# Performance work log

Hardware: AMD Instinct MI355X
Metric: run time of the kernel (lower is better)

The kernel has to match this reference:

```python
import jax, jax.numpy as jnp
import numpy as np

SOFTMAX = True
SPLAT = True


def setup_inputs() -> dict:
    key = jax.random.key(0)
    k1, k2 = jax.random.split(key)
    data = jax.random.normal(k1, (4, 3, 128, 128), dtype=jnp.float32)
    kernels = jax.random.normal(k2, (4, 441, 128, 128), dtype=jnp.float32)
    return {"data": data, "kernels": kernels}


def _scatter2gather(kern):
    # kern: [bs, k, k, h, w] splat kernels. Gather weight at pixel p for
    # neighbor offset d equals splat weight at pixel p+d for offset -d:
    #   gather[b,i,j,y,x] = splat[b, k-1-i, k-1-j, y+i-c, x+j-c]  (zero outside)
    bs, k, _, h, w = kern.shape
    c = k // 2
    flipped = kern[:, ::-1, ::-1]  # [bs,k,k,h,w]
    padded = jnp.pad(flipped, ((0, 0), (0, 0), (0, 0), (c, c), (c, c)))
    idx = jnp.arange(k)

    def slice_ij(i, j):
        plane = padded[:, i, j]  # [bs, h+2c, w+2c]
        return jax.lax.dynamic_slice(plane, (0, i, j), (bs, h, w))

    g = jax.vmap(lambda i: jax.vmap(lambda j: slice_ij(i, j))(idx))(idx)  # [k,k,bs,h,w]
    return jnp.transpose(g, (2, 0, 1, 3, 4))


def _kernel_weighting(data, kern):
    # out[b,c,y,x] = sum_ij kern[b,i,j,y,x] * data[b,c,y+i-cc,x+j-cc] (zero pad)
    # sum_w = same filtering applied to an all-ones tensor.
    bs, ch, h, w = data.shape
    k = kern.shape[1]
    cc = k // 2
    patches = jax.lax.conv_general_dilated_patches(
        data, (k, k), (1, 1), ((cc, cc), (cc, cc)))  # [bs, ch*k*k, h, w]
    patches = patches.reshape(bs, ch, k, k, h, w)
    out = jnp.einsum('bcijyx,bijyx->bcyx', patches, kern)
    # validity mask = zero-padded ones, separable in y/x
    ii = jnp.arange(k)
    yy = jnp.arange(h)
    xx = jnp.arange(w)
    py = yy[None, :] + ii[:, None] - cc  # [k,h]
    px = xx[None, :] + ii[:, None] - cc  # [k,w]
    vy = ((py >= 0) & (py < h))
    vx = ((px >= 0) & (px < w))
    valid = (vy[:, None, :, None] & vx[None, :, None, :]).astype(kern.dtype)  # [k,k,h,w]
    sum_w = jnp.einsum('bijyx,ijyx->byx', kern, valid)
    return out, sum_w


def reference(data, kernels):
    bs, k2, h, w = kernels.shape
    k = int(np.sqrt(k2))
    kern = kernels.reshape(bs, k, k, h, w)
    if SPLAT:
        kern = _scatter2gather(kern)
    if SOFTMAX:
        kern = jax.nn.softmax(kern.reshape(bs, k * k, h, w), axis=1)
        kern = kern.reshape(bs, k, k, h, w)
    out, sum_w = _kernel_weighting(data, kern)
    return out, sum_w[:, None]  # [bs,ch,h,w], [bs,1,h,w]
```

## Files before the change

kernel.cpp:

```cpp
#include <hip/hip_runtime.h>

#define KS 21
#define CC 10
#define H 128
#define W 128
#define HW (H*W)
#define NCH 3
#define B 4
#define PW (W + 2*CC)

typedef _Float16 half4v __attribute__((ext_vector_type(4)));
struct __attribute__((packed)) f4u { float v[4]; };

#define DT_BYTES (21*PW*8)

__global__ __launch_bounds__(256, 2)
void kaw_gather(const float* __restrict__ data,
                const float* __restrict__ kern,
                float* __restrict__ out,
                float* __restrict__ sumw)
{
    __shared__ __align__(16) unsigned char smem[DT_BYTES];
    unsigned char* dtB = smem;

    const int tid = threadIdx.x;
    const int w = tid & 7;
    const int t = tid >> 3;
    const int y = blockIdx.x;
    const int b = blockIdx.y;

    const float* __restrict__ kbase = kern + (size_t)b * (KS * KS) * HW;
    const float* __restrict__ dbase = data + (size_t)b * NCH * HW;

    for (int e = tid; e < 21 * PW; e += 256) {
        int r  = (e * 7085) >> 20;
        int c  = e - r * PW;
        int gy = y + r - CC;
        int gx = c - CC;
        half4v v = (half4v){(_Float16)0, (_Float16)0, (_Float16)0, (_Float16)0};
        if ((unsigned)gy < (unsigned)H && (unsigned)gx < (unsigned)W) {
            v.x = (_Float16)dbase[(0 * H + gy) * W + gx];
            v.y = (_Float16)dbase[(1 * H + gy) * W + gx];
            v.z = (_Float16)dbase[(2 * H + gy) * W + gx];
        }
        *reinterpret_cast<half4v*>(dtB + e * 8) = v;
    }
    __syncthreads();

    float a00 = 0.f, a01 = 0.f, a02 = 0.f, aw0 = 0.f;
    float a10 = 0.f, a11 = 0.f, a12 = 0.f, aw1 = 0.f;
    float a20 = 0.f, a21 = 0.f, a22 = 0.f, aw2 = 0.f;
    float a30 = 0.f, a31 = 0.f, a32 = 0.f, aw3 = 0.f;

    const int ntap = (w == 0) ? 56 : 55;
    int T = w;
    #pragma unroll 4
    for (int k = 0; k < ntap; ++k, T += 8) {
        int i  = (T * 3121) >> 16;
        int j  = T - i * 21;
        int py = y + i - CC;
        bool rv = (unsigned)py < (unsigned)H;
        int pyc = py < 0 ? 0 : (py > H - 1 ? H - 1 : py);
        int c0 = 4 * t + j - CC;
        f4u g = *reinterpret_cast<const f4u*>(
            kbase + (((440 - T) << 14) + (pyc << 7) + c0));
        float e0 = (rv && (unsigned)(c0 + 0) < (unsigned)W) ? __expf(g.v[0]) : 0.f;
        float e1 = (rv && (unsigned)(c0 + 1) < (unsigned)W) ? __expf(g.v[1]) : 0.f;
        float e2 = (rv && (unsigned)(c0 + 2) < (unsigned)W) ? __expf(g.v[2]) : 0.f;
        float e3 = (rv && (unsigned)(c0 + 3) < (unsigned)W) ? __expf(g.v[3]) : 0.f;
        const unsigned char* dp = dtB + (unsigned)(i * PW + c0 + CC) * 8;
        half4v d0 = *reinterpret_cast<const half4v*>(dp +  0);
        half4v d1 = *reinterpret_cast<const half4v*>(dp +  8);
        half4v d2 = *reinterpret_cast<const half4v*>(dp + 16);
        half4v d3 = *reinterpret_cast<const half4v*>(dp + 24);
        a00 += e0 * (float)d0.x; a01 += e0 * (float)d0.y; a02 += e0 * (float)d0.z; aw0 += e0;
        a10 += e1 * (float)d1.x; a11 += e1 * (float)d1.y; a12 += e1 * (float)d1.z; aw1 += e1;
        a20 += e2 * (float)d2.x; a21 += e2 * (float)d2.y; a22 += e2 * (float)d2.z; aw2 += e2;
        a30 += e3 * (float)d3.x; a31 += e3 * (float)d3.y; a32 += e3 * (float)d3.z; aw3 += e3;
    }

    __syncthreads();
    float4* sacc = (float4*)smem;
    sacc[w * 129 + 4 * t + 0] = make_float4(a00, a01, a02, aw0);
    sacc[w * 129 + 4 * t + 1] = make_float4(a10, a11, a12, aw1);
    sacc[w * 129 + 4 * t + 2] = make_float4(a20, a21, a22, aw2);
    sacc[w * 129 + 4 * t + 3] = make_float4(a30, a31, a32, aw3);
    __syncthreads();
    if (tid < W) {
        const int px = tid;
        float r0 = 0.f, r1 = 0.f, r2 = 0.f, rw = 0.f;
        #pragma unroll
        for (int s = 0; s < 8; ++s) {
            float4 p = sacc[s * 129 + px];
            r0 += p.x; r1 += p.y; r2 += p.z; rw += p.w;
        }
        int nry = max(0, CC - y)  + max(0, y  - (H - 1 - CC));
        int nrx = max(0, CC - px) + max(0, px - (W - 1 - CC));
        float co = 21.f * nry + (float)((21 - nry) * nrx);
        float inv = 1.0f / (rw + co);
        const size_t o = (size_t)b * NCH * HW + (size_t)y * W + px;
        out[o]          = r0 * inv;
        out[o + HW]     = r1 * inv;
        out[o + 2 * HW] = r2 * inv;
        sumw[(size_t)b * HW + (size_t)y * W + px] = rw * inv;
    }
}

extern "C" void kernel_launch(void* const* d_in, const int* in_sizes, int n_in,
                              void* d_out, int out_size, void* d_ws, size_t ws_size,
                              hipStream_t stream)
{
    const float* data = (const float*)d_in[0];
    const float* kern = (const float*)d_in[1];
    float* out  = (float*)d_out;
    float* sumw = out + (size_t)B * NCH * HW;

    dim3 g(H, B);
    kaw_gather<<<g, 256, 0, stream>>>(data, kern, out, sumw);
}
```

Measured before the change: 34.39 us.

## Split each row into two 64-pixel halves with 16 tap groups per block

Each block now handles half a row (64 pixels) instead of a full row, so the grid doubles. Taps are spread over 16 groups instead of 8, with incremental i/j/Q updates replacing the per-iteration division. Shared memory shrinks and launch bounds rise to 4 blocks per CU, aiming at more occupancy and more parallelism. In exchange the halo data tile is partly loaded twice, and the final reduction has to sum 16 partial results instead of 8.

New measurement: 30.66 us. 1.12x faster.

```diff
diff --git a/kernel.cpp b/kernel.cpp
--- a/kernel.cpp
+++ b/kernel.cpp
@@ -7,36 +7,38 @@
 #define HW (H*W)
 #define NCH 3
 #define B 4
-#define PW (W + 2*CC)
+#define HWX 64
+#define PWX (HWX + 2*CC)
 
 typedef _Float16 half4v __attribute__((ext_vector_type(4)));
 struct __attribute__((packed)) f4u { float v[4]; };
 
-#define DT_BYTES (21*PW*8)
+#define SMEM_BYTES (16*65*16)
 
-__global__ __launch_bounds__(256, 2)
+__global__ __launch_bounds__(256, 4)
 void kaw_gather(const float* __restrict__ data,
                 const float* __restrict__ kern,
                 float* __restrict__ out,
                 float* __restrict__ sumw)
 {
-    __shared__ __align__(16) unsigned char smem[DT_BYTES];
+    __shared__ __align__(16) unsigned char smem[SMEM_BYTES];
     unsigned char* dtB = smem;
 
     const int tid = threadIdx.x;
-    const int w = tid & 7;
-    const int t = tid >> 3;
-    const int y = blockIdx.x;
-    const int b = blockIdx.y;
+    const int w  = tid >> 4;
+    const int t  = tid & 15;
+    const int y  = blockIdx.x;
+    const int x0 = blockIdx.y * HWX;
+    const int b  = blockIdx.z;
 
     const float* __restrict__ kbase = kern + (size_t)b * (KS * KS) * HW;
     const float* __restrict__ dbase = data + (size_t)b * NCH * HW;
 
-    for (int e = tid; e < 21 * PW; e += 256) {
-        int r  = (e * 7085) >> 20;
-        int c  = e - r * PW;
+    for (int e = tid; e < 21 * PWX; e += 256) {
+        int r  = e / PWX;
+        int c  = e - r * PWX;
         int gy = y + r - CC;
-        int gx = c - CC;
+        int gx = x0 + c - CC;
         half4v v = (half4v){(_Float16)0, (_Float16)0, (_Float16)0, (_Float16)0};
         if ((unsigned)gy < (unsigned)H && (unsigned)gx < (unsigned)W) {
             v.x = (_Float16)dbase[(0 * H + gy) * W + gx];
@@ -52,23 +54,21 @@
     float a20 = 0.f, a21 = 0.f, a22 = 0.f, aw2 = 0.f;
     float a30 = 0.f, a31 = 0.f, a32 = 0.f, aw3 = 0.f;
 
-    const int ntap = (w == 0) ? 56 : 55;
-    int T = w;
+    const int ntap = (w <= 8) ? 28 : 27;
+    int i = 0, j = w, Q = 440 - w;
     #pragma unroll 4
-    for (int k = 0; k < ntap; ++k, T += 8) {
-        int i  = (T * 3121) >> 16;
-        int j  = T - i * 21;
+    for (int k = 0; k < ntap; ++k) {
         int py = y + i - CC;
         bool rv = (unsigned)py < (unsigned)H;
         int pyc = py < 0 ? 0 : (py > H - 1 ? H - 1 : py);
-        int c0 = 4 * t + j - CC;
+        int c0 = x0 + 4 * t + j - CC;
         f4u g = *reinterpret_cast<const f4u*>(
-            kbase + (((440 - T) << 14) + (pyc << 7) + c0));
+            kbase + ((Q << 14) + (pyc << 7) + c0));
         float e0 = (rv && (unsigned)(c0 + 0) < (unsigned)W) ? __expf(g.v[0]) : 0.f;
         float e1 = (rv && (unsigned)(c0 + 1) < (unsigned)W) ? __expf(g.v[1]) : 0.f;
         float e2 = (rv && (unsigned)(c0 + 2) < (unsigned)W) ? __expf(g.v[2]) : 0.f;
         float e3 = (rv && (unsigned)(c0 + 3) < (unsigned)W) ? __expf(g.v[3]) : 0.f;
-        const unsigned char* dp = dtB + (unsigned)(i * PW + c0 + CC) * 8;
+        const unsigned char* dp = dtB + (unsigned)(i * PWX + 4 * t + j) * 8;
         half4v d0 = *reinterpret_cast<const half4v*>(dp +  0);
         half4v d1 = *reinterpret_cast<const half4v*>(dp +  8);
         half4v d2 = *reinterpret_cast<const half4v*>(dp + 16);
@@ -77,21 +77,24 @@
         a10 += e1 * (float)d1.x; a11 += e1 * (float)d1.y; a12 += e1 * (float)d1.z; aw1 += e1;
         a20 += e2 * (float)d2.x; a21 += e2 * (float)d2.y; a22 += e2 * (float)d2.z; aw2 += e2;
         a30 += e3 * (float)d3.x; a31 += e3 * (float)d3.y; a32 += e3 * (float)d3.z; aw3 += e3;
+        j += 16; Q -= 16;
+        if (j >= KS) { j -= KS; ++i; }
     }
 
     __syncthreads();
     float4* sacc = (float4*)smem;
-    sacc[w * 129 + 4 * t + 0] = make_float4(a00, a01, a02, aw0);
-    sacc[w * 129 + 4 * t + 1] = make_float4(a10, a11, a12, aw1);
-    sacc[w * 129 + 4 * t + 2] = make_float4(a20, a21, a22, aw2);
-    sacc[w * 129 + 4 * t + 3] = make_float4(a30, a31, a32, aw3);
+    sacc[w * 65 + 4 * t + 0] = make_float4(a00, a01, a02, aw0);
+    sacc[w * 65 + 4 * t + 1] = make_float4(a10, a11, a12, aw1);
+    sacc[w * 65 + 4 * t + 2] = make_float4(a20, a21, a22, aw2);
+    sacc[w * 65 + 4 * t + 3] = make_float4(a30, a31, a32, aw3);
     __syncthreads();
-    if (tid < W) {
-        const int px = tid;
+    if (tid < HWX) {
+        const int lp = tid;
+        const int px = x0 + lp;
         float r0 = 0.f, r1 = 0.f, r2 = 0.f, rw = 0.f;
         #pragma unroll
-        for (int s = 0; s < 8; ++s) {
-            float4 p = sacc[s * 129 + px];
+        for (int s = 0; s < 16; ++s) {
+            float4 p = sacc[s * 65 + lp];
             r0 += p.x; r1 += p.y; r2 += p.z; rw += p.w;
         }
         int nry = max(0, CC - y)  + max(0, y  - (H - 1 - CC));
@@ -115,6 +118,6 @@
     float* out  = (float*)d_out;
     float* sumw = out + (size_t)B * NCH * HW;
 
-    dim3 g(H, B);
+    dim3 g(H, 2, B);
     kaw_gather<<<g, 256, 0, stream>>>(data, kern, out, sumw);
 }
```

## Use 512-thread blocks, mask padding via ones channel, incremental tap indexing

Applied to the files above, without the earlier changes.

Doubles the block to 512 threads, splitting the 441 taps across 16 wave-groups instead of 8, so each thread handles about 28 taps. The per-tap validity checks are removed: padded positions carry a fourth half channel set to 1 for valid pixels and 0 otherwise, and that channel also gates the weight sum. Tap indices are now advanced incrementally, which drops the per-iteration divide-by-multiply. The cost is more shared memory for the 16-way reduction and a larger block that may limit occupancy. Exponentials of clamped or out-of-range kernel values are still computed and only masked by the zeroed data.

Result: faster. 29.76 us, median of 2 (-13.5%).

```diff
diff --git a/kernel.cpp b/kernel.cpp
--- a/kernel.cpp
+++ b/kernel.cpp
@@ -12,28 +12,28 @@
 typedef _Float16 half4v __attribute__((ext_vector_type(4)));
 struct __attribute__((packed)) f4u { float v[4]; };
 
-#define DT_BYTES (21*PW*8)
+#define SMEM_BYTES (16*129*16)
 
-__global__ __launch_bounds__(256, 2)
+__global__ __launch_bounds__(512, 2)
 void kaw_gather(const float* __restrict__ data,
                 const float* __restrict__ kern,
                 float* __restrict__ out,
                 float* __restrict__ sumw)
 {
-    __shared__ __align__(16) unsigned char smem[DT_BYTES];
+    __shared__ __align__(16) unsigned char smem[SMEM_BYTES];
     unsigned char* dtB = smem;
 
     const int tid = threadIdx.x;
-    const int w = tid & 7;
-    const int t = tid >> 3;
+    const int t = tid & 31;
+    const int w = tid >> 5;
     const int y = blockIdx.x;
     const int b = blockIdx.y;
 
     const float* __restrict__ kbase = kern + (size_t)b * (KS * KS) * HW;
     const float* __restrict__ dbase = data + (size_t)b * NCH * HW;
 
-    for (int e = tid; e < 21 * PW; e += 256) {
-        int r  = (e * 7085) >> 20;
+    for (int e = tid; e < 21 * PW; e += 512) {
+        int r  = e / PW;
         int c  = e - r * PW;
         int gy = y + r - CC;
         int gx = c - CC;
@@ -42,6 +42,7 @@
             v.x = (_Float16)dbase[(0 * H + gy) * W + gx];
             v.y = (_Float16)dbase[(1 * H + gy) * W + gx];
             v.z = (_Float16)dbase[(2 * H + gy) * W + gx];
+            v.w = (_Float16)1.0f;
         }
         *reinterpret_cast<half4v*>(dtB + e * 8) = v;
     }
@@ -52,31 +53,30 @@
     float a20 = 0.f, a21 = 0.f, a22 = 0.f, aw2 = 0.f;
     float a30 = 0.f, a31 = 0.f, a32 = 0.f, aw3 = 0.f;
 
-    const int ntap = (w == 0) ? 56 : 55;
-    int T = w;
+    const int ntap = (w < 9) ? 28 : 27;
+    int i = 0, j = w, Q = 440 - w;
     #pragma unroll 4
-    for (int k = 0; k < ntap; ++k, T += 8) {
-        int i  = (T * 3121) >> 16;
-        int j  = T - i * 21;
-        int py = y + i - CC;
-        bool rv = (unsigned)py < (unsigned)H;
+    for (int k = 0; k < ntap; ++k) {
+        int py  = y + i - CC;
         int pyc = py < 0 ? 0 : (py > H - 1 ? H - 1 : py);
-        int c0 = 4 * t + j - CC;
+        int c0  = 4 * t + j - CC;
         f4u g = *reinterpret_cast<const f4u*>(
-            kbase + (((440 - T) << 14) + (pyc << 7) + c0));
-        float e0 = (rv && (unsigned)(c0 + 0) < (unsigned)W) ? __expf(g.v[0]) : 0.f;
-        float e1 = (rv && (unsigned)(c0 + 1) < (unsigned)W) ? __expf(g.v[1]) : 0.f;
-        float e2 = (rv && (unsigned)(c0 + 2) < (unsigned)W) ? __expf(g.v[2]) : 0.f;
-        float e3 = (rv && (unsigned)(c0 + 3) < (unsigned)W) ? __expf(g.v[3]) : 0.f;
-        const unsigned char* dp = dtB + (unsigned)(i * PW + c0 + CC) * 8;
+            kbase + ((Q << 14) + (pyc << 7) + c0));
+        float e0 = __expf(g.v[0]);
+        float e1 = __expf(g.v[1]);
+        float e2 = __expf(g.v[2]);
+        float e3 = __expf(g.v[3]);
+        const unsigned char* dp = dtB + (unsigned)(i * PW + 4 * t + j) * 8;
         half4v d0 = *reinterpret_cast<const half4v*>(dp +  0);
         half4v d1 = *reinterpret_cast<const half4v*>(dp +  8);
         half4v d2 = *reinterpret_cast<const half4v*>(dp + 16);
         half4v d3 = *reinterpret_cast<const half4v*>(dp + 24);
-        a00 += e0 * (float)d0.x; a01 += e0 * (float)d0.y; a02 += e0 * (float)d0.z; aw0 += e0;
-        a10 += e1 * (float)d1.x; a11 += e1 * (float)d1.y; a12 += e1 * (float)d1.z; aw1 += e1;
-        a20 += e2 * (float)d2.x; a21 += e2 * (float)d2.y; a22 += e2 * (float)d2.z; aw2 += e2;
-        a30 += e3 * (float)d3.x; a31 += e3 * (float)d3.y; a32 += e3 * (float)d3.z; aw3 += e3;
+        a00 += e0 * (float)d0.x; a01 += e0 * (float)d0.y; a02 += e0 * (float)d0.z; aw0 += e0 * (float)d0.w;
+        a10 += e1 * (float)d1.x; a11 += e1 * (float)d1.y; a12 += e1 * (float)d1.z; aw1 += e1 * (float)d1.w;
+        a20 += e2 * (float)d2.x; a21 += e2 * (float)d2.y; a22 += e2 * (float)d2.z; aw2 += e2 * (float)d2.w;
+        a30 += e3 * (float)d3.x; a31 += e3 * (float)d3.y; a32 += e3 * (float)d3.z; aw3 += e3 * (float)d3.w;
+        j += 16; Q -= 16;
+        if (j >= KS) { j -= KS; ++i; }
     }
 
     __syncthreads();
@@ -90,7 +90,7 @@
         const int px = tid;
         float r0 = 0.f, r1 = 0.f, r2 = 0.f, rw = 0.f;
         #pragma unroll
-        for (int s = 0; s < 8; ++s) {
+        for (int s = 0; s < 16; ++s) {
             float4 p = sacc[s * 129 + px];
             r0 += p.x; r1 += p.y; r2 += p.z; rw += p.w;
         }
@@ -116,5 +116,5 @@
     float* sumw = out + (size_t)B * NCH * HW;
 
     dim3 g(H, B);
-    kaw_gather<<<g, 256, 0, stream>>>(data, kern, out, sumw);
+    kaw_gather<<<g, 512, 0, stream>>>(data, kern, out, sumw);
 }
```
